# Performance work log

Measured on AMD Instinct MI355X. Metric: run time of the kernel, lower is better.

The kernel has to match this reference:

```python
import jax, jax.numpy as jnp
import numpy as np
import math

B, NO, L = 128, 100, 36
VS, TS, D, H, NB = 2048, 1024, 1024, 8, 2
DH = D // H
SCALE = 1.0 / math.sqrt(DH)


def _shape(x):
    # [B, N, D] -> [B, H, N, DH]
    b, n, _ = x.shape
    return x.reshape(b, n, H, DH).transpose(0, 2, 1, 3)


def _unshape(x):
    # [B, H, N, DH] -> [B, N, D]
    return x.transpose(0, 2, 1, 3).reshape(x.shape[0], x.shape[2], D)


def _masked_softmax(scores, key_mask):
    # scores [B,H,Nq,Nk]; key_mask [B,Nk] float (1=valid, 0=pad)
    scores = jnp.where(key_mask[:, None, None, :] > 0, scores, -jnp.inf)
    return jax.nn.softmax(scores, axis=-1)


def _forward(v, t, vm, tm,
             vlin_w, vlin_b, tlin_w, tlin_b,
             iv_w, iv_b, it_w, it_b, ivo_w, ivo_b, ito_w, ito_b,
             gv_w, gv_b, gt_w, gt_b, av_w, av_b, at_w, at_b,
             avo_w, avo_b, ato_w, ato_b):
    # initial projection to hidden size (dropout is identity at drop=0.0)
    v = v @ vlin_w + vlin_b
    t = t @ tlin_w + tlin_b
    for _ in range(NB):  # weights shared across blocks (SingleBlock)
        # ---- InterModalityUpdate ----
        v = v * vm[..., None]
        t = t * tm[..., None]
        vt = jax.nn.relu(v) @ iv_w + iv_b   # [B,NO,3D]
        tt = jax.nn.relu(t) @ it_w + it_b   # [B,L,3D]
        vk, vq, vv = [_shape(a) for a in jnp.split(vt, 3, axis=2)]
        tk, tq, tv = [_shape(a) for a in jnp.split(tt, 3, axis=2)]
        t2v = _masked_softmax(jnp.einsum('bhnd,bhmd->bhnm', vq, tk) * SCALE, tm)
        v2t = _masked_softmax(jnp.einsum('bhnd,bhmd->bhnm', tq, vk) * SCALE, vm)
        v_up = _unshape(jnp.einsum('bhnm,bhmd->bhnd', t2v, tv))
        t_up = _unshape(jnp.einsum('bhnm,bhmd->bhnd', v2t, vv))
        v = jnp.concatenate([v, v_up], axis=2) @ ivo_w + ivo_b
        t = jnp.concatenate([t, t_up], axis=2) @ ito_w + ito_b
        # ---- DyIntraModalityUpdate ----
        v_mean = (v * vm[..., None]).sum(1) / vm.sum(1, keepdims=True)  # [B,D]
        t_mean = (t * tm[..., None]).sum(1) / tm.sum(1, keepdims=True)
        v4t_gate = jax.nn.sigmoid(jax.nn.relu(v_mean) @ gv_w + gv_b)  # gates text
        t4v_gate = jax.nn.sigmoid(jax.nn.relu(t_mean) @ gt_w + gt_b)  # gates vision
        gate_t = (1.0 + v4t_gate).reshape(-1, H, 1, DH)  # [B,H,1,DH]
        gate_v = (1.0 + t4v_gate).reshape(-1, H, 1, DH)
        vt2 = (jax.nn.relu(v) @ av_w + av_b) * vm[..., None]
        tt2 = (jax.nn.relu(t) @ at_w + at_b) * tm[..., None]
        vk2, vq2, vv2 = [_shape(a) for a in jnp.split(vt2, 3, axis=2)]
        tk2, tq2, tv2 = [_shape(a) for a in jnp.split(tt2, 3, axis=2)]
        v2v = _masked_softmax(jnp.einsum('bhnd,bhmd->bhnm', gate_v * vq2, gate_v * vk2) * SCALE, vm)
        t2t = _masked_softmax(jnp.einsum('bhnd,bhmd->bhnm', gate_t * tq2, gate_t * tk2) * SCALE, tm)
        v_up2 = _unshape(jnp.einsum('bhnm,bhmd->bhnd', v2v, vv2))
        t_up2 = _unshape(jnp.einsum('bhnm,bhmd->bhnd', t2t, tv2))
        v = (v + v_up2) @ avo_w + avo_b
        t = (t + t_up2) @ ato_w + ato_b
    return v, t


def setup_inputs() -> dict:
    key = jax.random.key(0)
    ks = list(jax.random.split(key, 20))
    WS = 0.02  # weight init scale

    def rn(k, shape, s=1.0):
        return jax.random.normal(k, shape, dtype=jnp.float32) * s

    inp = {
        'v': rn(ks[0], (B, NO, VS)),
        't': rn(ks[1], (B, L, TS)),
        'v_mask': jnp.ones((B, NO), dtype=jnp.float32),
        't_mask': jnp.ones((B, L), dtype=jnp.float32),
        'vlin_w': rn(ks[2], (VS, D), WS), 'vlin_b': jnp.zeros((D,), jnp.float32),
        'tlin_w': rn(ks[3], (TS, D), WS), 'tlin_b': jnp.zeros((D,), jnp.float32),
        'iv_w': rn(ks[4], (D, 3 * D), WS), 'iv_b': jnp.zeros((3 * D,), jnp.float32),
        'it_w': rn(ks[5], (D, 3 * D), WS), 'it_b': jnp.zeros((3 * D,), jnp.float32),
        'ivo_w': rn(ks[6], (2 * D, D), WS), 'ivo_b': jnp.zeros((D,), jnp.float32),
        'ito_w': rn(ks[7], (2 * D, D), WS), 'ito_b': jnp.zeros((D,), jnp.float32),
        'gv_w': rn(ks[8], (D, D), WS), 'gv_b': jnp.zeros((D,), jnp.float32),
        'gt_w': rn(ks[9], (D, D), WS), 'gt_b': jnp.zeros((D,), jnp.float32),
        'av_w': rn(ks[10], (D, 3 * D), WS), 'av_b': jnp.zeros((3 * D,), jnp.float32),
        'at_w': rn(ks[11], (D, 3 * D), WS), 'at_b': jnp.zeros((3 * D,), jnp.float32),
        'avo_w': rn(ks[12], (D, D), WS), 'avo_b': jnp.zeros((D,), jnp.float32),
        'ato_w': rn(ks[13], (D, D), WS), 'ato_b': jnp.zeros((D,), jnp.float32),
    }
    return inp


def reference(v, t, v_mask, t_mask,
              vlin_w, vlin_b, tlin_w, tlin_b,
              iv_w, iv_b, it_w, it_b, ivo_w, ivo_b, ito_w, ito_b,
              gv_w, gv_b, gt_w, gt_b, av_w, av_b, at_w, at_b,
              avo_w, avo_b, ato_w, ato_b):
    return _forward(v, t, v_mask, t_mask,
                    vlin_w, vlin_b, tlin_w, tlin_b,
                    iv_w, iv_b, it_w, it_b, ivo_w, ivo_b, ito_w, ito_b,
                    gv_w, gv_b, gt_w, gt_b, av_w, av_b, at_w, at_b,
                    avo_w, avo_b, ato_w, ato_b)
```

## Files before the change

### kernel.cpp

```cpp
#include <hip/hip_runtime.h>

typedef __bf16 bf16x8 __attribute__((ext_vector_type(8)));
typedef float f32x4 __attribute__((ext_vector_type(4)));

#define SCALEF 0.08838834764831843f
#define FL_RELU 1
#define FL_SIG 2

__device__ __forceinline__ float bf2f(short u) {
    unsigned int x = ((unsigned int)(unsigned short)u) << 16;
    return __builtin_bit_cast(float, x);
}
__device__ __forceinline__ short f2bf(float f) {
    unsigned int x = __builtin_bit_cast(unsigned int, f);
    unsigned int r = (x + 0x7FFFu + ((x >> 16) & 1u)) >> 16;
    return (short)(unsigned short)r;
}
__device__ __forceinline__ unsigned int pkbf(float lo, float hi) {
    return ((unsigned int)(unsigned short)f2bf(lo)) | (((unsigned int)(unsigned short)f2bf(hi)) << 16);
}
__device__ __forceinline__ unsigned int relu_pk(unsigned int p) {
    unsigned int sgn = p & 0x80008000u;
    unsigned int m = (sgn >> 15) * 0xFFFFu;
    return p & ~m;
}
__device__ __forceinline__ void gload16(const void* g, void* l) {
    __builtin_amdgcn_global_load_lds(
        (const __attribute__((address_space(1))) unsigned int*)g,
        (__attribute__((address_space(3))) unsigned int*)l, 16, 0, 0);
}

template<int RELU, int CF32>
__global__ __launch_bounds__(256, 4) void gemm_k(
    const short* __restrict__ A1, const short* __restrict__ A2, int k2s, int lda,
    const short* __restrict__ WT, const float* __restrict__ bias,
    const float* __restrict__ rmask, void* __restrict__ Cv,
    int M, int N, int K, int ldc, int flags)
{
    __shared__ short lA[128 * 64];
    __shared__ short lB[128 * 64];
    const int tid = threadIdx.x;
    const int lane = tid & 63;
    const int wave = tid >> 6;
    const int wr = wave >> 1, wc = wave & 1;
    const int q16 = lane & 15, gk = lane >> 4;

    const int nbx = gridDim.x;
    const int nwg = nbx * gridDim.y;
    int orig = blockIdx.y * nbx + blockIdx.x;
    int qq = nwg >> 3, rr = nwg & 7;
    int xcd = orig & 7, idx = orig >> 3;
    int swz = (xcd < rr ? xcd * (qq + 1) : rr * (qq + 1) + (xcd - rr) * qq) + idx;
    const int bn = (swz % nbx) * 128;
    const int bm = (swz / nbx) * 128;

    const int srow = lane >> 3;
    const int scol = ((lane & 7) ^ srow) * 8;

    f32x4 acc[4][4];
#pragma unroll
    for (int i = 0; i < 4; ++i)
#pragma unroll
        for (int j = 0; j < 4; ++j) acc[i][j] = (f32x4){0.f, 0.f, 0.f, 0.f};

    for (int k0 = 0; k0 < K; k0 += 64) {
        const short* Asrc = A1; int kc = k0;
        if (A2 != nullptr && k0 >= k2s) { Asrc = A2; kc = k0 - k2s; }
#pragma unroll
        for (int i = 0; i < 4; ++i) {
            int chunk = wave * 4 + i;
            int row = chunk * 8 + srow;
            gload16(Asrc + (size_t)(bm + row) * lda + kc + scol, lA + chunk * 512);
            gload16(WT + (size_t)(bn + row) * K + k0 + scol, lB + chunk * 512);
        }
        __syncthreads();
#pragma unroll
        for (int kk = 0; kk < 2; ++kk) {
            bf16x8 af[4], bfr[4];
#pragma unroll
            for (int i = 0; i < 4; ++i) {
                int row = wr * 64 + i * 16 + q16;
                int off = (row * 128 + kk * 64 + gk * 16) ^ ((row & 7) << 4);
                af[i] = *(const bf16x8*)((const char*)lA + off);
                if (RELU) {
                    union { bf16x8 v; unsigned int w[4]; } u;
                    u.v = af[i];
#pragma unroll
                    for (int t = 0; t < 4; ++t) u.w[t] = relu_pk(u.w[t]);
                    af[i] = u.v;
                }
            }
#pragma unroll
            for (int j = 0; j < 4; ++j) {
                int row = wc * 64 + j * 16 + q16;
                int off = (row * 128 + kk * 64 + gk * 16) ^ ((row & 7) << 4);
                bfr[j] = *(const bf16x8*)((const char*)lB + off);
            }
#pragma unroll
            for (int i = 0; i < 4; ++i)
#pragma unroll
                for (int j = 0; j < 4; ++j)
                    acc[i][j] = __builtin_amdgcn_mfma_f32_16x16x32_bf16(af[i], bfr[j], acc[i][j], 0, 0, 0);
        }
        __syncthreads();
    }
    const bool sig = (flags & FL_SIG) != 0;
#pragma unroll
    for (int i = 0; i < 4; ++i) {
#pragma unroll
        for (int j = 0; j < 4; ++j) {
            int col = bn + wc * 64 + j * 16 + q16;
            float bv = bias[col];
#pragma unroll
            for (int r = 0; r < 4; ++r) {
                int row = bm + wr * 64 + i * 16 + gk * 4 + r;
                float v = acc[i][j][r] + bv;
                if (sig) v = 1.f + 1.f / (1.f + __expf(-v));
                if (rmask) v *= rmask[row];
                if (CF32) ((float*)Cv)[(size_t)row * ldc + col] = v;
                else      ((short*)Cv)[(size_t)row * ldc + col] = f2bf(v);
            }
        }
    }
}

template<int KT>
__global__ __launch_bounds__(256, 2) void attn_mfma(
    const short* __restrict__ qsrc, const short* __restrict__ kvsrc,
    const float* __restrict__ maskp, const short* __restrict__ gate,
    const short* __restrict__ addsrc,
    short* __restrict__ outp, int Nq, int Nk)
{
    constexpr int KT2 = (KT + 1) / 2;
    constexpr int KROWS = KT * 16;
    constexpr int KV = KT2 * 32;
    constexpr int VROWB = KV * 2;
    __shared__ short sK[KROWS * 128];
    __shared__ short sVT[128 * KV];
    __shared__ float sMask[KV];

    const int tid = threadIdx.x;
    const int h = blockIdx.x, b = blockIdx.y;
    const int lane = tid & 63, w = tid >> 6;
    const int g = lane >> 4, q16 = lane & 15;

    union U8 { uint4 u4; short s[8]; };

    for (int u = tid; u < Nk * 16; u += 256) {
        int k = u >> 4, seg = u & 15;
        U8 t; t.u4 = *(const uint4*)(kvsrc + (size_t)(b * Nk + k) * 3072 + h * 128 + seg * 8);
        if (gate) {
            const short* gp = gate + b * 1024 + h * 128 + seg * 8;
#pragma unroll
            for (int j = 0; j < 8; ++j) {
                float gv = bf2f(gp[j]);
                t.s[j] = f2bf(bf2f(t.s[j]) * gv * gv);
            }
        }
        int off = (k * 256 + seg * 16) ^ ((k & 7) << 4);
        *(uint4*)((char*)sK + off) = t.u4;
    }
    for (int u = tid; u < Nk * 16; u += 256) {
        int k = u >> 4, seg = u & 15;
        U8 t; t.u4 = *(const uint4*)(kvsrc + (size_t)(b * Nk + k) * 3072 + 2048 + h * 128 + seg * 8);
#pragma unroll
        for (int j = 0; j < 8; ++j) {
            int d = seg * 8 + j;
            int off = (d * VROWB + ((k >> 3) << 4) + (k & 7) * 2) ^ ((d & 7) << 4);
            *(short*)((char*)sVT + off) = t.s[j];
        }
    }
    for (int u = tid; u < (KV - Nk) * 128; u += 256) {
        int k = Nk + (u >> 7), d = u & 127;
        int off = (d * VROWB + ((k >> 3) << 4) + (k & 7) * 2) ^ ((d & 7) << 4);
        *(short*)((char*)sVT + off) = 0;
    }
    for (int u = tid; u < KV; u += 256)
        sMask[u] = (u < Nk) ? maskp[b * Nk + u] : 0.f;
    __syncthreads();

    const int QT = (Nq + 15) >> 4;
    for (int qt = w; qt < QT; qt += 4) {
        int qrow = qt * 16 + q16; if (qrow >= Nq) qrow = Nq - 1;
        const short* qp = qsrc + (size_t)(b * Nq + qrow) * 3072 + 1024 + h * 128 + g * 8;
        bf16x8 qf[4];
#pragma unroll
        for (int ks = 0; ks < 4; ++ks)
            qf[ks] = *(const bf16x8*)(qp + ks * 32);

        f32x4 accs[KT];
#pragma unroll
        for (int kt = 0; kt < KT; ++kt) accs[kt] = (f32x4){0.f, 0.f, 0.f, 0.f};
#pragma unroll
        for (int kt = 0; kt < KT; ++kt) {
            int krow = kt * 16 + q16;
#pragma unroll
            for (int ks = 0; ks < 4; ++ks) {
                bf16x8 kf = *(const bf16x8*)((char*)sK +
                    ((krow * 256 + ks * 64 + g * 16) ^ ((krow & 7) << 4)));
                accs[kt] = __builtin_amdgcn_mfma_f32_16x16x32_bf16(kf, qf[ks], accs[kt], 0, 0, 0);
            }
        }
        float pv[KT][4];
        float mx = -__builtin_inff();
#pragma unroll
        for (int kt = 0; kt < KT; ++kt)
#pragma unroll
            for (int r = 0; r < 4; ++r) {
                int k = kt * 16 + g * 4 + r;
                float s = (sMask[k] > 0.f) ? accs[kt][r] * SCALEF : -__builtin_inff();
                pv[kt][r] = s;
                mx = fmaxf(mx, s);
            }
        mx = fmaxf(mx, __shfl_xor(mx, 16, 64));
        mx = fmaxf(mx, __shfl_xor(mx, 32, 64));
        float sum = 0.f;
#pragma unroll
        for (int kt = 0; kt < KT; ++kt)
#pragma unroll
            for (int r = 0; r < 4; ++r) {
                float p = __expf(pv[kt][r] - mx);
                pv[kt][r] = p;
                sum += p;
            }
        sum += __shfl_xor(sum, 16, 64);
        sum += __shfl_xor(sum, 32, 64);
        float rden = 1.f / sum;

        unsigned int wA[KT2 * 2], wB[KT2 * 2];
#pragma unroll
        for (int t = 0; t < KT2 * 2; ++t) {
            if (t < KT) { wA[t] = pkbf(pv[t][0], pv[t][1]); wB[t] = pkbf(pv[t][2], pv[t][3]); }
            else { wA[t] = 0u; wB[t] = 0u; }
        }
        f32x4 acco[8];
#pragma unroll
        for (int dt = 0; dt < 8; ++dt) acco[dt] = (f32x4){0.f, 0.f, 0.f, 0.f};
        const int srcA = (((g & 1) * 2) * 16 + q16) * 4;
        const int srcB = (((g & 1) * 2 + 1) * 16 + q16) * 4;
        const bool hi = g >= 2;
#pragma unroll
        for (int kt2 = 0; kt2 < KT2; ++kt2) {
            int a0 = __builtin_amdgcn_ds_bpermute(srcA, (int)wA[2 * kt2]);
            int a1 = __builtin_amdgcn_ds_bpermute(srcA, (int)wA[2 * kt2 + 1]);
            int b0 = __builtin_amdgcn_ds_bpermute(srcA, (int)wB[2 * kt2]);
            int b1 = __builtin_amdgcn_ds_bpermute(srcA, (int)wB[2 * kt2 + 1]);
            int c0 = __builtin_amdgcn_ds_bpermute(srcB, (int)wA[2 * kt2]);
            int c1 = __builtin_amdgcn_ds_bpermute(srcB, (int)wA[2 * kt2 + 1]);
            int d0 = __builtin_amdgcn_ds_bpermute(srcB, (int)wB[2 * kt2]);
            int d1 = __builtin_amdgcn_ds_bpermute(srcB, (int)wB[2 * kt2 + 1]);
            union { int wd[4]; bf16x8 v; } pf;
            pf.wd[0] = hi ? a1 : a0;
            pf.wd[1] = hi ? b1 : b0;
            pf.wd[2] = hi ? c1 : c0;
            pf.wd[3] = hi ? d1 : d0;
#pragma unroll
            for (int dt = 0; dt < 8; ++dt) {
                int drow = dt * 16 + q16;
                bf16x8 vf = *(const bf16x8*)((char*)sVT +
                    ((drow * VROWB + kt2 * 64 + g * 16) ^ ((drow & 7) << 4)));
                acco[dt] = __builtin_amdgcn_mfma_f32_16x16x32_bf16(pf.v, vf, acco[dt], 0, 0, 0);
            }
        }
        float rd[4];
#pragma unroll
        for (int r = 0; r < 4; ++r) {
            int rv = __builtin_amdgcn_ds_bpermute((g * 4 + r) * 4, __builtin_bit_cast(int, rden));
            rd[r] = __builtin_bit_cast(float, rv);
        }
#pragma unroll
        for (int dt = 0; dt < 8; ++dt)
#pragma unroll
            for (int r = 0; r < 4; ++r) {
                int q = qt * 16 + g * 4 + r;
                if (q < Nq) {
                    size_t oidx = (size_t)(b * Nq + q) * 1024 + h * 128 + dt * 16 + q16;
                    float val = acco[dt][r] * rd[r];
                    if (addsrc) val += bf2f(addsrc[oidx]);
                    outp[oidx] = f2bf(val);
                }
            }
    }
}

__global__ void transpose_k(const float* __restrict__ W, short* __restrict__ WT, int K, int N) {
    __shared__ short tile[32][33];
    int nb = blockIdx.x * 32, kb = blockIdx.y * 32;
    int tx = threadIdx.x & 31, ty = threadIdx.x >> 5;
    for (int i = ty; i < 32; i += 8)
        tile[i][tx] = f2bf(W[(size_t)(kb + i) * N + nb + tx]);
    __syncthreads();
    for (int i = ty; i < 32; i += 8)
        WT[(size_t)(nb + i) * K + kb + tx] = tile[tx][i];
}

__global__ void cvt_bf(const float* __restrict__ in, short* __restrict__ out, int n8) {
    int i = blockIdx.x * 256 + threadIdx.x;
    if (i >= n8) return;
    const float4* p = (const float4*)(in + (size_t)i * 8);
    float4 x = p[0], y = p[1];
    uint4 val;
    val.x = pkbf(x.x, x.y); val.y = pkbf(x.z, x.w);
    val.z = pkbf(y.x, y.y); val.w = pkbf(y.z, y.w);
    *(uint4*)(out + (size_t)i * 8) = val;
}

__global__ void mean_k(const short* __restrict__ X, const float* __restrict__ mask,
                       short* __restrict__ outp, int N) {
    int idx = blockIdx.x * 256 + threadIdx.x;
    int b = idx >> 10, d = idx & 1023;
    float s = 0.f, c = 0.f;
    for (int n = 0; n < N; ++n) {
        float mv = mask[b * N + n];
        s += bf2f(X[(size_t)(b * N + n) * 1024 + d]) * mv;
        c += mv;
    }
    outp[idx] = f2bf(s / c);
}

extern "C" void kernel_launch(void* const* d_in, const int* in_sizes, int n_in,
                              void* d_out, int out_size, void* d_ws, size_t ws_size,
                              hipStream_t stream)
{
    const float* v_in  = (const float*)d_in[0];
    const float* t_in  = (const float*)d_in[1];
    const float* vm    = (const float*)d_in[2];
    const float* tm    = (const float*)d_in[3];
    const float* vlin_w = (const float*)d_in[4];  const float* vlin_b = (const float*)d_in[5];
    const float* tlin_w = (const float*)d_in[6];  const float* tlin_b = (const float*)d_in[7];
    const float* iv_w  = (const float*)d_in[8];   const float* iv_b  = (const float*)d_in[9];
    const float* it_w  = (const float*)d_in[10];  const float* it_b  = (const float*)d_in[11];
    const float* ivo_w = (const float*)d_in[12];  const float* ivo_b = (const float*)d_in[13];
    const float* ito_w = (const float*)d_in[14];  const float* ito_b = (const float*)d_in[15];
    const float* gv_w  = (const float*)d_in[16];  const float* gv_b  = (const float*)d_in[17];
    const float* gt_w  = (const float*)d_in[18];  const float* gt_b  = (const float*)d_in[19];
    const float* av_w  = (const float*)d_in[20];  const float* av_b  = (const float*)d_in[21];
    const float* at_w  = (const float*)d_in[22];  const float* at_b  = (const float*)d_in[23];
    const float* avo_w = (const float*)d_in[24];  const float* avo_b = (const float*)d_in[25];
    const float* ato_w = (const float*)d_in[26];  const float* ato_b = (const float*)d_in[27];

    short* ws = (short*)d_ws;
    const size_t WTvlin = 0;
    const size_t WTtlin = 2097152;
    const size_t WTiv   = 3145728;
    const size_t WTit   = 6291456;
    const size_t WTivo  = 9437184;
    const size_t WTito  = 11534336;
    const size_t WTgv   = 13631488;
    const size_t WTgt   = 14680064;
    const size_t WTav   = 15728640;
    const size_t WTat   = 18874368;
    const size_t WTavo  = 22020096;
    const size_t WTato  = 23068672;
    const size_t V_A    = 24117248;
    const size_t V_B    = 37224448;
    const size_t T_A    = 50331648;
    const size_t T_B    = 55050240;
    const size_t VT     = 59768832;
    const size_t TT     = 99090432;
    const size_t V_UP   = 113246208;
    const size_t T_UP   = 126353408;
    const size_t VMEAN  = 131072000;
    const size_t TMEAN  = 131203072;
    const size_t GATEV  = 131334144;
    const size_t GATET  = 131465216;
    const size_t TOTAL  = 131596288;
    if (ws_size < TOTAL * 2ull) return;

    auto T = [&](const float* W, size_t WToff, int K, int N) {
        dim3 g(N / 32, K / 32);
        transpose_k<<<g, 256, 0, stream>>>(W, ws + WToff, K, N);
    };
    auto G = [&](const short* A1, const short* A2, int k2s, int lda,
                 size_t WToff, const float* bp, const float* rm,
                 short* Cp, int M, int N, int K, int flags) {
        dim3 g(N / 128, M / 128);
        if (flags & FL_RELU)
            gemm_k<1, 0><<<g, 256, 0, stream>>>(A1, A2, k2s, lda, ws + WToff, bp, rm, Cp, M, N, K, N, flags);
        else
            gemm_k<0, 0><<<g, 256, 0, stream>>>(A1, A2, k2s, lda, ws + WToff, bp, rm, Cp, M, N, K, N, flags);
    };
    auto GO = [&](const short* A1, int lda, size_t WToff, const float* bp,
                  float* Cp, int M, int N, int K) {
        dim3 g(N / 128, M / 128);
        gemm_k<0, 1><<<g, 256, 0, stream>>>(A1, nullptr, 0, lda, ws + WToff, bp, nullptr, Cp, M, N, K, N, 0);
    };
    auto ATT = [&](const short* q, const short* kv, const float* mk, const short* gt,
                   const short* adds, short* o, int Nq, int Nk) {
        dim3 g(8, 128);
        if (Nk > 48)
            attn_mfma<7><<<g, 256, 0, stream>>>(q, kv, mk, gt, adds, o, Nq, Nk);
        else
            attn_mfma<3><<<g, 256, 0, stream>>>(q, kv, mk, gt, adds, o, Nq, Nk);
    };

    T(vlin_w, WTvlin, 2048, 1024);  T(tlin_w, WTtlin, 1024, 1024);
    T(iv_w, WTiv, 1024, 3072);      T(it_w, WTit, 1024, 3072);
    T(ivo_w, WTivo, 2048, 1024);    T(ito_w, WTito, 2048, 1024);
    T(gv_w, WTgv, 1024, 1024);      T(gt_w, WTgt, 1024, 1024);
    T(av_w, WTav, 1024, 3072);      T(at_w, WTat, 1024, 3072);
    T(avo_w, WTavo, 1024, 1024);    T(ato_w, WTato, 1024, 1024);

    short* v_a = ws + V_A; short* v_b = ws + V_B;
    short* t_a = ws + T_A; short* t_b = ws + T_B;
    short* vt = ws + VT;   short* tt = ws + TT;
    short* v_up = ws + V_UP; short* t_up = ws + T_UP;
    short* vmean = ws + VMEAN; short* tmean = ws + TMEAN;
    short* gateV = ws + GATEV; short* gateT = ws + GATET;
    float* ov = (float*)d_out;
    float* ot = ov + 13107200;

    {
        short* v_cv = ws + VT;
        short* t_cv = ws + TT;
        cvt_bf<<<(12800 * 2048 / 8 + 255) / 256, 256, 0, stream>>>(v_in, v_cv, 12800 * 2048 / 8);
        cvt_bf<<<(4608 * 1024 / 8 + 255) / 256, 256, 0, stream>>>(t_in, t_cv, 4608 * 1024 / 8);
        G(v_cv, nullptr, 0, 2048, WTvlin, vlin_b, vm, v_a, 12800, 1024, 2048, 0);
        G(t_cv, nullptr, 0, 1024, WTtlin, tlin_b, tm, t_a, 4608, 1024, 1024, 0);
    }

    for (int ib = 0; ib < 2; ++ib) {
        G(v_a, nullptr, 0, 1024, WTiv, iv_b, nullptr, vt, 12800, 3072, 1024, FL_RELU);
        G(t_a, nullptr, 0, 1024, WTit, it_b, nullptr, tt, 4608, 3072, 1024, FL_RELU);
        ATT(vt, tt, tm, nullptr, nullptr, v_up, 100, 36);
        ATT(tt, vt, vm, nullptr, nullptr, t_up, 36, 100);
        G(v_a, v_up, 1024, 1024, WTivo, ivo_b, nullptr, v_b, 12800, 1024, 2048, 0);
        G(t_a, t_up, 1024, 1024, WTito, ito_b, nullptr, t_b, 4608, 1024, 2048, 0);
        mean_k<<<512, 256, 0, stream>>>(v_b, vm, vmean, 100);
        mean_k<<<512, 256, 0, stream>>>(t_b, tm, tmean, 36);
        G(vmean, nullptr, 0, 1024, WTgv, gv_b, nullptr, gateT, 128, 1024, 1024, FL_RELU | FL_SIG);
        G(tmean, nullptr, 0, 1024, WTgt, gt_b, nullptr, gateV, 128, 1024, 1024, FL_RELU | FL_SIG);
        G(v_b, nullptr, 0, 1024, WTav, av_b, vm, vt, 12800, 3072, 1024, FL_RELU);
        G(t_b, nullptr, 0, 1024, WTat, at_b, tm, tt, 4608, 3072, 1024, FL_RELU);
        ATT(vt, vt, vm, gateV, v_b, v_up, 100, 100);
        ATT(tt, tt, tm, gateT, t_b, t_up, 36, 36);
        if (ib == 1) {
            GO(v_up, 1024, WTavo, avo_b, ov, 12800, 1024, 1024);
            GO(t_up, 1024, WTato, ato_b, ot, 4608, 1024, 1024);
        } else {
            G(v_up, nullptr, 0, 1024, WTavo, avo_b, vm, v_a, 12800, 1024, 1024, 0);
            G(t_up, nullptr, 0, 1024, WTato, ato_b, tm, t_a, 4608, 1024, 1024, 0);
        }
    }
}
```

Before: 1.823 ms.

## Batch paired vision/text launches into single grouped kernels via blockIdx.z

Merges each vision/text pair of GEMM, attention, mean and convert launches into one launch that selects its parameter struct by blockIdx.z. The twelve weight transposes also become a single packed launch. This cuts launch count and lets the smaller text work fill the GPU alongside the vision work instead of running in its own tail. In exchange, the text half of each grid launches 100 rows of blocks that mostly exit at once, and attention now always uses the KT=7 variant, wasting work on the short 36-key cases.

```diff
diff --git a/kernel.cpp b/kernel.cpp
--- a/kernel.cpp
+++ b/kernel.cpp
@@ -4,7 +4,6 @@
 typedef float f32x4 __attribute__((ext_vector_type(4)));
 
 #define SCALEF 0.08838834764831843f
-#define FL_RELU 1
 #define FL_SIG 2
 
 __device__ __forceinline__ float bf2f(short u) {
@@ -30,13 +29,20 @@
         (__attribute__((address_space(3))) unsigned int*)l, 16, 0, 0);
 }
 
+struct GP {
+    const short* A1; const short* A2; const short* WT;
+    const float* bias; const float* rmask; void* C;
+    int k2s, lda, M, N, K, ldc, flags;
+};
+
 template<int RELU, int CF32>
-__global__ __launch_bounds__(256, 4) void gemm_k(
-    const short* __restrict__ A1, const short* __restrict__ A2, int k2s, int lda,
-    const short* __restrict__ WT, const float* __restrict__ bias,
-    const float* __restrict__ rmask, void* __restrict__ Cv,
-    int M, int N, int K, int ldc, int flags)
+__global__ __launch_bounds__(256, 4) void gemm2_k(GP p0, GP p1)
 {
+    GP p = (blockIdx.z == 0) ? p0 : p1;
+    const int nbx = p.N >> 7;
+    const int nby = p.M >> 7;
+    if ((int)blockIdx.y >= nby) return;
+
     __shared__ short lA[128 * 64];
     __shared__ short lB[128 * 64];
     const int tid = threadIdx.x;
@@ -45,8 +51,7 @@
     const int wr = wave >> 1, wc = wave & 1;
     const int q16 = lane & 15, gk = lane >> 4;
 
-    const int nbx = gridDim.x;
-    const int nwg = nbx * gridDim.y;
+    const int nwg = nbx * nby;
     int orig = blockIdx.y * nbx + blockIdx.x;
     int qq = nwg >> 3, rr = nwg & 7;
     int xcd = orig & 7, idx = orig >> 3;
@@ -63,15 +68,15 @@
 #pragma unroll
         for (int j = 0; j < 4; ++j) acc[i][j] = (f32x4){0.f, 0.f, 0.f, 0.f};
 
-    for (int k0 = 0; k0 < K; k0 += 64) {
-        const short* Asrc = A1; int kc = k0;
-        if (A2 != nullptr && k0 >= k2s) { Asrc = A2; kc = k0 - k2s; }
+    for (int k0 = 0; k0 < p.K; k0 += 64) {
+        const short* Asrc = p.A1; int kc = k0;
+        if (p.A2 != nullptr && k0 >= p.k2s) { Asrc = p.A2; kc = k0 - p.k2s; }
 #pragma unroll
         for (int i = 0; i < 4; ++i) {
             int chunk = wave * 4 + i;
             int row = chunk * 8 + srow;
-            gload16(Asrc + (size_t)(bm + row) * lda + kc + scol, lA + chunk * 512);
-            gload16(WT + (size_t)(bn + row) * K + k0 + scol, lB + chunk * 512);
+            gload16(Asrc + (size_t)(bm + row) * p.lda + kc + scol, lA + chunk * 512);
+            gload16(p.WT + (size_t)(bn + row) * p.K + k0 + scol, lB + chunk * 512);
         }
         __syncthreads();
 #pragma unroll
@@ -104,34 +109,34 @@
         }
         __syncthreads();
     }
-    const bool sig = (flags & FL_SIG) != 0;
+    const bool sig = (p.flags & FL_SIG) != 0;
 #pragma unroll
     for (int i = 0; i < 4; ++i) {
 #pragma unroll
         for (int j = 0; j < 4; ++j) {
             int col = bn + wc * 64 + j * 16 + q16;
-            float bv = bias[col];
+            float bv = p.bias[col];
 #pragma unroll
             for (int r = 0; r < 4; ++r) {
                 int row = bm + wr * 64 + i * 16 + gk * 4 + r;
                 float v = acc[i][j][r] + bv;
                 if (sig) v = 1.f + 1.f / (1.f + __expf(-v));
-                if (rmask) v *= rmask[row];
-                if (CF32) ((float*)Cv)[(size_t)row * ldc + col] = v;
-                else      ((short*)Cv)[(size_t)row * ldc + col] = f2bf(v);
-            }
-        }
-    }
-}
-
-template<int KT>
-__global__ __launch_bounds__(256, 2) void attn_mfma(
-    const short* __restrict__ qsrc, const short* __restrict__ kvsrc,
-    const float* __restrict__ maskp, const short* __restrict__ gate,
-    const short* __restrict__ addsrc,
-    short* __restrict__ outp, int Nq, int Nk)
+                if (p.rmask) v *= p.rmask[row];
+                if (CF32) ((float*)p.C)[(size_t)row * p.ldc + col] = v;
+                else      ((short*)p.C)[(size_t)row * p.ldc + col] = f2bf(v);
+            }
+        }
+    }
+}
+
+struct AP {
+    const short* q; const short* kv; const float* mask; const short* gate;
+    const short* add; short* out; int Nq, Nk;
+};
+
+__global__ __launch_bounds__(256, 2) void attn2_mfma(AP a0, AP a1)
 {
-    constexpr int KT2 = (KT + 1) / 2;
+    constexpr int KT = 7, KT2 = 4;
     constexpr int KROWS = KT * 16;
     constexpr int KV = KT2 * 32;
     constexpr int VROWB = KV * 2;
@@ -139,6 +144,8 @@
     __shared__ short sVT[128 * KV];
     __shared__ float sMask[KV];
 
+    AP a = (blockIdx.z == 0) ? a0 : a1;
+    const int Nq = a.Nq, Nk = a.Nk;
     const int tid = threadIdx.x;
     const int h = blockIdx.x, b = blockIdx.y;
     const int lane = tid & 63, w = tid >> 6;
@@ -148,9 +155,9 @@
 
     for (int u = tid; u < Nk * 16; u += 256) {
         int k = u >> 4, seg = u & 15;
-        U8 t; t.u4 = *(const uint4*)(kvsrc + (size_t)(b * Nk + k) * 3072 + h * 128 + seg * 8);
-        if (gate) {
-            const short* gp = gate + b * 1024 + h * 128 + seg * 8;
+        U8 t; t.u4 = *(const uint4*)(a.kv + (size_t)(b * Nk + k) * 3072 + h * 128 + seg * 8);
+        if (a.gate) {
+            const short* gp = a.gate + b * 1024 + h * 128 + seg * 8;
 #pragma unroll
             for (int j = 0; j < 8; ++j) {
                 float gv = bf2f(gp[j]);
@@ -162,7 +169,7 @@
     }
     for (int u = tid; u < Nk * 16; u += 256) {
         int k = u >> 4, seg = u & 15;
-        U8 t; t.u4 = *(const uint4*)(kvsrc + (size_t)(b * Nk + k) * 3072 + 2048 + h * 128 + seg * 8);
+        U8 t; t.u4 = *(const uint4*)(a.kv + (size_t)(b * Nk + k) * 3072 + 2048 + h * 128 + seg * 8);
 #pragma unroll
         for (int j = 0; j < 8; ++j) {
             int d = seg * 8 + j;
@@ -176,13 +183,13 @@
         *(short*)((char*)sVT + off) = 0;
     }
     for (int u = tid; u < KV; u += 256)
-        sMask[u] = (u < Nk) ? maskp[b * Nk + u] : 0.f;
+        sMask[u] = (u < Nk) ? a.mask[b * Nk + u] : 0.f;
     __syncthreads();
 
     const int QT = (Nq + 15) >> 4;
     for (int qt = w; qt < QT; qt += 4) {
         int qrow = qt * 16 + q16; if (qrow >= Nq) qrow = Nq - 1;
-        const short* qp = qsrc + (size_t)(b * Nq + qrow) * 3072 + 1024 + h * 128 + g * 8;
+        const short* qp = a.q + (size_t)(b * Nq + qrow) * 3072 + 1024 + h * 128 + g * 8;
         bf16x8 qf[4];
 #pragma unroll
         for (int ks = 0; ks < 4; ++ks)
@@ -241,19 +248,19 @@
         const bool hi = g >= 2;
 #pragma unroll
         for (int kt2 = 0; kt2 < KT2; ++kt2) {
-            int a0 = __builtin_amdgcn_ds_bpermute(srcA, (int)wA[2 * kt2]);
-            int a1 = __builtin_amdgcn_ds_bpermute(srcA, (int)wA[2 * kt2 + 1]);
-            int b0 = __builtin_amdgcn_ds_bpermute(srcA, (int)wB[2 * kt2]);
-            int b1 = __builtin_amdgcn_ds_bpermute(srcA, (int)wB[2 * kt2 + 1]);
-            int c0 = __builtin_amdgcn_ds_bpermute(srcB, (int)wA[2 * kt2]);
-            int c1 = __builtin_amdgcn_ds_bpermute(srcB, (int)wA[2 * kt2 + 1]);
-            int d0 = __builtin_amdgcn_ds_bpermute(srcB, (int)wB[2 * kt2]);
-            int d1 = __builtin_amdgcn_ds_bpermute(srcB, (int)wB[2 * kt2 + 1]);
+            int a0_ = __builtin_amdgcn_ds_bpermute(srcA, (int)wA[2 * kt2]);
+            int a1_ = __builtin_amdgcn_ds_bpermute(srcA, (int)wA[2 * kt2 + 1]);
+            int b0_ = __builtin_amdgcn_ds_bpermute(srcA, (int)wB[2 * kt2]);
+            int b1_ = __builtin_amdgcn_ds_bpermute(srcA, (int)wB[2 * kt2 + 1]);
+            int c0_ = __builtin_amdgcn_ds_bpermute(srcB, (int)wA[2 * kt2]);
+            int c1_ = __builtin_amdgcn_ds_bpermute(srcB, (int)wA[2 * kt2 + 1]);
+            int d0_ = __builtin_amdgcn_ds_bpermute(srcB, (int)wB[2 * kt2]);
+            int d1_ = __builtin_amdgcn_ds_bpermute(srcB, (int)wB[2 * kt2 + 1]);
             union { int wd[4]; bf16x8 v; } pf;
-            pf.wd[0] = hi ? a1 : a0;
-            pf.wd[1] = hi ? b1 : b0;
-            pf.wd[2] = hi ? c1 : c0;
-            pf.wd[3] = hi ? d1 : d0;
+            pf.wd[0] = hi ? a1_ : a0_;
+            pf.wd[1] = hi ? b1_ : b0_;
+            pf.wd[2] = hi ? c1_ : c0_;
+            pf.wd[3] = hi ? d1_ : d0_;
 #pragma unroll
             for (int dt = 0; dt < 8; ++dt) {
                 int drow = dt * 16 + q16;
@@ -276,16 +283,26 @@
                 if (q < Nq) {
                     size_t oidx = (size_t)(b * Nq + q) * 1024 + h * 128 + dt * 16 + q16;
                     float val = acco[dt][r] * rd[r];
-                    if (addsrc) val += bf2f(addsrc[oidx]);
-                    outp[oidx] = f2bf(val);
+                    if (a.add) val += bf2f(a.add[oidx]);
+                    a.out[oidx] = f2bf(val);
                 }
             }
     }
 }
 
-__global__ void transpose_k(const float* __restrict__ W, short* __restrict__ WT, int K, int N) {
+struct TP { const float* W; short* WT; int K, N, nblk; };
+struct TPack { TP t[12]; };
+
+__global__ void transpose12_k(TPack pk) {
     __shared__ short tile[32][33];
-    int nb = blockIdx.x * 32, kb = blockIdx.y * 32;
+    int bid = blockIdx.x;
+    int pi = 0;
+    while (bid >= pk.t[pi].nblk) { bid -= pk.t[pi].nblk; ++pi; }
+    const float* W = pk.t[pi].W;
+    short* WT = pk.t[pi].WT;
+    int K = pk.t[pi].K, N = pk.t[pi].N;
+    int nbx = N >> 5;
+    int nb = (bid % nbx) * 32, kb = (bid / nbx) * 32;
     int tx = threadIdx.x & 31, ty = threadIdx.x >> 5;
     for (int i = ty; i < 32; i += 8)
         tile[i][tx] = f2bf(W[(size_t)(kb + i) * N + nb + tx]);
@@ -294,28 +311,35 @@
         WT[(size_t)(nb + i) * K + kb + tx] = tile[tx][i];
 }
 
-__global__ void cvt_bf(const float* __restrict__ in, short* __restrict__ out, int n8) {
+__global__ void cvt2_bf(const float* __restrict__ a, short* __restrict__ oa, int na8,
+                        const float* __restrict__ b, short* __restrict__ ob, int nb8) {
     int i = blockIdx.x * 256 + threadIdx.x;
-    if (i >= n8) return;
-    const float4* p = (const float4*)(in + (size_t)i * 8);
+    const float* src; short* dst; int loc;
+    if (i < na8) { src = a; dst = oa; loc = i; }
+    else if (i < na8 + nb8) { src = b; dst = ob; loc = i - na8; }
+    else return;
+    const float4* p = (const float4*)(src + (size_t)loc * 8);
     float4 x = p[0], y = p[1];
     uint4 val;
     val.x = pkbf(x.x, x.y); val.y = pkbf(x.z, x.w);
     val.z = pkbf(y.x, y.y); val.w = pkbf(y.z, y.w);
-    *(uint4*)(out + (size_t)i * 8) = val;
-}
-
-__global__ void mean_k(const short* __restrict__ X, const float* __restrict__ mask,
-                       short* __restrict__ outp, int N) {
+    *(uint4*)(dst + (size_t)loc * 8) = val;
+}
+
+__global__ void mean2_k(const short* __restrict__ Xv, const float* __restrict__ mv, short* __restrict__ ov_,
+                        const short* __restrict__ Xt, const float* __restrict__ mt, short* __restrict__ ot_) {
     int idx = blockIdx.x * 256 + threadIdx.x;
-    int b = idx >> 10, d = idx & 1023;
+    const short* X; const float* mk; short* o; int N; int loc;
+    if (idx < 131072) { X = Xv; mk = mv; o = ov_; N = 100; loc = idx; }
+    else { X = Xt; mk = mt; o = ot_; N = 36; loc = idx - 131072; }
+    int b = loc >> 10, d = loc & 1023;
     float s = 0.f, c = 0.f;
     for (int n = 0; n < N; ++n) {
-        float mv = mask[b * N + n];
-        s += bf2f(X[(size_t)(b * N + n) * 1024 + d]) * mv;
-        c += mv;
-    }
-    outp[idx] = f2bf(s / c);
+        float m = mk[b * N + n];
+        s += bf2f(X[(size_t)(b * N + n) * 1024 + d]) * m;
+        c += m;
+    }
+    o[loc] = f2bf(s / c);
 }
 
 extern "C" void kernel_launch(void* const* d_in, const int* in_sizes, int n_in,
@@ -367,40 +391,6 @@
     const size_t TOTAL  = 131596288;
     if (ws_size < TOTAL * 2ull) return;
 
-    auto T = [&](const float* W, size_t WToff, int K, int N) {
-        dim3 g(N / 32, K / 32);
-        transpose_k<<<g, 256, 0, stream>>>(W, ws + WToff, K, N);
-    };
-    auto G = [&](const short* A1, const short* A2, int k2s, int lda,
-                 size_t WToff, const float* bp, const float* rm,
-                 short* Cp, int M, int N, int K, int flags) {
-        dim3 g(N / 128, M / 128);
-        if (flags & FL_RELU)
-            gemm_k<1, 0><<<g, 256, 0, stream>>>(A1, A2, k2s, lda, ws + WToff, bp, rm, Cp, M, N, K, N, flags);
-        else
-            gemm_k<0, 0><<<g, 256, 0, stream>>>(A1, A2, k2s, lda, ws + WToff, bp, rm, Cp, M, N, K, N, flags);
-    };
-    auto GO = [&](const short* A1, int lda, size_t WToff, const float* bp,
-                  float* Cp, int M, int N, int K) {
-        dim3 g(N / 128, M / 128);
-        gemm_k<0, 1><<<g, 256, 0, stream>>>(A1, nullptr, 0, lda, ws + WToff, bp, nullptr, Cp, M, N, K, N, 0);
-    };
-    auto ATT = [&](const short* q, const short* kv, const float* mk, const short* gt,
-                   const short* adds, short* o, int Nq, int Nk) {
-        dim3 g(8, 128);
-        if (Nk > 48)
-            attn_mfma<7><<<g, 256, 0, stream>>>(q, kv, mk, gt, adds, o, Nq, Nk);
-        else
-            attn_mfma<3><<<g, 256, 0, stream>>>(q, kv, mk, gt, adds, o, Nq, Nk);
-    };
-
-    T(vlin_w, WTvlin, 2048, 1024);  T(tlin_w, WTtlin, 1024, 1024);
-    T(iv_w, WTiv, 1024, 3072);      T(it_w, WTit, 1024, 3072);
-    T(ivo_w, WTivo, 2048, 1024);    T(ito_w, WTito, 2048, 1024);
-    T(gv_w, WTgv, 1024, 1024);      T(gt_w, WTgt, 1024, 1024);
-    T(av_w, WTav, 1024, 3072);      T(at_w, WTat, 1024, 3072);
-    T(avo_w, WTavo, 1024, 1024);    T(ato_w, WTato, 1024, 1024);
-
     short* v_a = ws + V_A; short* v_b = ws + V_B;
     short* t_a = ws + T_A; short* t_b = ws + T_B;
     short* vt = ws + VT;   short* tt = ws + TT;
@@ -411,35 +401,68 @@
     float* ot = ov + 13107200;
 
     {
+        TPack pk;
+        auto set = [&](int i, const float* W, size_t off, int K, int N) {
+            pk.t[i] = TP{W, ws + off, K, N, (N / 32) * (K / 32)};
+        };
+        set(0, vlin_w, WTvlin, 2048, 1024);  set(1, tlin_w, WTtlin, 1024, 1024);
+        set(2, iv_w, WTiv, 1024, 3072);      set(3, it_w, WTit, 1024, 3072);
+        set(4, ivo_w, WTivo, 2048, 1024);    set(5, ito_w, WTito, 2048, 1024);
+        set(6, gv_w, WTgv, 1024, 1024);      set(7, gt_w, WTgt, 1024, 1024);
+        set(8, av_w, WTav, 1024, 3072);      set(9, at_w, WTat, 1024, 3072);
+        set(10, avo_w, WTavo, 1024, 1024);   set(11, ato_w, WTato, 1024, 1024);
+        int total = 0;
+        for (int i = 0; i < 12; ++i) total += pk.t[i].nblk;
+        transpose12_k<<<total, 256, 0, stream>>>(pk);
+    }
+
+    auto GPm = [&](const short* A1, const short* A2, int k2s, int lda, size_t WToff,
+                   const float* bp, const float* rm, void* Cp, int M, int N, int K, int flags) {
+        return GP{A1, A2, ws + WToff, bp, rm, Cp, k2s, lda, M, N, K, N, flags};
+    };
+    auto APm = [&](const short* q, const short* kv, const float* mk, const short* gt,
+                   const short* adds, short* o, int Nq, int Nk) {
+        return AP{q, kv, mk, gt, adds, o, Nq, Nk};
+    };
+
+    {
         short* v_cv = ws + VT;
         short* t_cv = ws + TT;
-        cvt_bf<<<(12800 * 2048 / 8 + 255) / 256, 256, 0, stream>>>(v_in, v_cv, 12800 * 2048 / 8);
-        cvt_bf<<<(4608 * 1024 / 8 + 255) / 256, 256, 0, stream>>>(t_in, t_cv, 4608 * 1024 / 8);
-        G(v_cv, nullptr, 0, 2048, WTvlin, vlin_b, vm, v_a, 12800, 1024, 2048, 0);
-        G(t_cv, nullptr, 0, 1024, WTtlin, tlin_b, tm, t_a, 4608, 1024, 1024, 0);
+        int na8 = 12800 * 2048 / 8, nb8 = 4608 * 1024 / 8;
+        cvt2_bf<<<(na8 + nb8 + 255) / 256, 256, 0, stream>>>(v_in, v_cv, na8, t_in, t_cv, nb8);
+        gemm2_k<0, 0><<<dim3(8, 100, 2), 256, 0, stream>>>(
+            GPm(v_cv, nullptr, 0, 2048, WTvlin, vlin_b, vm, v_a, 12800, 1024, 2048, 0),
+            GPm(t_cv, nullptr, 0, 1024, WTtlin, tlin_b, tm, t_a, 4608, 1024, 1024, 0));
     }
 
     for (int ib = 0; ib < 2; ++ib) {
-        G(v_a, nullptr, 0, 1024, WTiv, iv_b, nullptr, vt, 12800, 3072, 1024, FL_RELU);
-        G(t_a, nullptr, 0, 1024, WTit, it_b, nullptr, tt, 4608, 3072, 1024, FL_RELU);
-        ATT(vt, tt, tm, nullptr, nullptr, v_up, 100, 36);
-        ATT(tt, vt, vm, nullptr, nullptr, t_up, 36, 100);
-        G(v_a, v_up, 1024, 1024, WTivo, ivo_b, nullptr, v_b, 12800, 1024, 2048, 0);
-        G(t_a, t_up, 1024, 1024, WTito, ito_b, nullptr, t_b, 4608, 1024, 2048, 0);
-        mean_k<<<512, 256, 0, stream>>>(v_b, vm, vmean, 100);
-        mean_k<<<512, 256, 0, stream>>>(t_b, tm, tmean, 36);
-        G(vmean, nullptr, 0, 1024, WTgv, gv_b, nullptr, gateT, 128, 1024, 1024, FL_RELU | FL_SIG);
-        G(tmean, nullptr, 0, 1024, WTgt, gt_b, nullptr, gateV, 128, 1024, 1024, FL_RELU | FL_SIG);
-        G(v_b, nullptr, 0, 1024, WTav, av_b, vm, vt, 12800, 3072, 1024, FL_RELU);
-        G(t_b, nullptr, 0, 1024, WTat, at_b, tm, tt, 4608, 3072, 1024, FL_RELU);
-        ATT(vt, vt, vm, gateV, v_b, v_up, 100, 100);
-        ATT(tt, tt, tm, gateT, t_b, t_up, 36, 36);
+        gemm2_k<1, 0><<<dim3(24, 100, 2), 256, 0, stream>>>(
+            GPm(v_a, nullptr, 0, 1024, WTiv, iv_b, nullptr, vt, 12800, 3072, 1024, 0),
+            GPm(t_a, nullptr, 0, 1024, WTit, it_b, nullptr, tt, 4608, 3072, 1024, 0));
+        attn2_mfma<<<dim3(8, 128, 2), 256, 0, stream>>>(
+            APm(vt, tt, tm, nullptr, nullptr, v_up, 100, 36),
+            APm(tt, vt, vm, nullptr, nullptr, t_up, 36, 100));
+        gemm2_k<0, 0><<<dim3(8, 100, 2), 256, 0, stream>>>(
+            GPm(v_a, v_up, 1024, 1024, WTivo, ivo_b, nullptr, v_b, 12800, 1024, 2048, 0),
+            GPm(t_a, t_up, 1024, 1024, WTito, ito_b, nullptr, t_b, 4608, 1024, 2048, 0));
+        mean2_k<<<1024, 256, 0, stream>>>(v_b, vm, vmean, t_b, tm, tmean);
+        gemm2_k<1, 0><<<dim3(8, 1, 2), 256, 0, stream>>>(
+            GPm(vmean, nullptr, 0, 1024, WTgv, gv_b, nullptr, gateT, 128, 1024, 1024, FL_SIG),
+            GPm(tmean, nullptr, 0, 1024, WTgt, gt_b, nullptr, gateV, 128, 1024, 1024, FL_SIG));
+        gemm2_k<1, 0><<<dim3(24, 100, 2), 256, 0, stream>>>(
+            GPm(v_b, nullptr, 0, 1024, WTav, av_b, vm, vt, 12800, 3072, 1024, 0),
+            GPm(t_b, nullptr, 0, 1024, WTat, at_b, tm, tt, 4608, 3072, 1024, 0));
+        attn2_mfma<<<dim3(8, 128, 2), 256, 0, stream>>>(
+            APm(vt, vt, vm, gateV, v_b, v_up, 100, 100),
+            APm(tt, tt, tm, gateT, t_b, t_up, 36, 36));
         if (ib == 1) {
-            GO(v_up, 1024, WTavo, avo_b, ov, 12800, 1024, 1024);
-            GO(t_up, 1024, WTato, ato_b, ot, 4608, 1024, 1024);
+            gemm2_k<0, 1><<<dim3(8, 100, 2), 256, 0, stream>>>(
+                GPm(v_up, nullptr, 0, 1024, WTavo, avo_b, nullptr, ov, 12800, 1024, 1024, 0),
+                GPm(t_up, nullptr, 0, 1024, WTato, ato_b, nullptr, ot, 4608, 1024, 1024, 0));
         } else {
-            G(v_up, nullptr, 0, 1024, WTavo, avo_b, vm, v_a, 12800, 1024, 1024, 0);
-            G(t_up, nullptr, 0, 1024, WTato, ato_b, tm, t_a, 4608, 1024, 1024, 0);
-        }
-    }
-}
+            gemm2_k<0, 0><<<dim3(8, 100, 2), 256, 0, stream>>>(
+                GPm(v_up, nullptr, 0, 1024, WTavo, avo_b, vm, v_a, 12800, 1024, 1024, 0),
+                GPm(t_up, nullptr, 0, 1024, WTato, ato_b, tm, t_a, 4608, 1024, 1024, 0));
+        }
+    }
+}
```

New measurement: 1.702 ms. -6.6%, faster.
